# Optimization experiments

Hardware: AMD Instinct MI355X
Metric: run time of the kernel (lower is better)

Reference implementation:

```python
import jax, jax.numpy as jnp
import numpy as np

N_SERIES = 100000
INPUT_SIZE = 28
OUTPUT_SIZE = 7
N_T = 1
N_S = 4
PERIOD = 7            # seasonality = [7]
EMBED = 1 + 1 + PERIOD  # lev_sms, seas_sms, init seasonal factors
BATCH = 2048
N_TIME = 2048


def setup_inputs() -> dict:
    key = jax.random.key(0)
    k1, k2, k3, k4 = jax.random.split(key, 4)
    # Y must be strictly positive (multiplicative model: division + log)
    Y = jax.random.uniform(k1, (BATCH, N_TIME), dtype=jnp.float32, minval=0.5, maxval=1.5)
    X = jax.random.normal(k2, (BATCH, N_T, N_TIME), dtype=jnp.float32)
    S = jax.random.normal(k3, (BATCH, N_S), dtype=jnp.float32)
    idxs = jax.random.randint(k4, (BATCH,), 0, N_SERIES)
    embeds_weight = jnp.full((N_SERIES, EMBED), 0.5, dtype=jnp.float32)
    return {"S": S, "Y": Y, "X": X, "idxs": idxs,
            "embeds_weight": embeds_weight, "step_size": 7}


def _levels_seasons(Y, idxs, embeds_weight):
    """Exponential smoothing level/seasonality recurrence (single seasonality)."""
    emb = embeds_weight[idxs]                      # (B, 9)
    lev_sms = jax.nn.sigmoid(emb[:, 0])            # (B,)
    seas_sms = jax.nn.sigmoid(emb[:, 1])           # (B,)
    init_seas = jnp.exp(emb[:, 2:2 + PERIOD])      # (B, 7)

    level0 = Y[:, 0] / init_seas[:, 0]
    # ring buffer holding the seasonal factors used at steps t=1..: [s1..s6, s0]
    buf0 = jnp.concatenate([init_seas[:, 1:], init_seas[:, :1]], axis=1)  # (B, 7)

    def step(carry, inp):
        lev, buf = carry
        y, k = inp
        s = jnp.take(buf, k % PERIOD, axis=1)                       # seasonality at lag PERIOD
        newlev = lev_sms * (y / s) + (1.0 - lev_sms) * lev
        news = seas_sms * (y / newlev) + (1.0 - seas_sms) * s
        buf = jax.lax.dynamic_update_slice_in_dim(buf, news[:, None], k % PERIOD, axis=1)
        return (newlev, buf), (newlev, news)

    ks = jnp.arange(N_TIME - 1, dtype=jnp.int32)
    (_, _), (levs, seas) = jax.lax.scan(step, (level0, buf0), (Y[:, 1:].T, ks))
    levels = jnp.concatenate([level0[:, None], levs.T], axis=1)           # (B, n_time)
    seasonal = jnp.concatenate([init_seas, init_seas[:, :1], seas.T], axis=1)  # (B, n_time+7)
    return levels, seasonal


def reference(S, Y, X, idxs, embeds_weight, step_size):
    levels, seasonal = _levels_seasons(Y, idxs, embeds_weight)

    windows_end = N_TIME - INPUT_SIZE - OUTPUT_SIZE + 1
    windows = np.arange(0, windows_end, step_size)          # static window starts
    W = len(windows)

    # --- insample windows, normalized: log(Y / level / season) ---
    idx_in = windows[:, None] + np.arange(INPUT_SIZE)       # (W, I)
    Yw = Y[:, idx_in]                                       # (B, W, I)
    lev_w = levels[:, windows + INPUT_SIZE - 1]             # (B, W)
    seas_w = seasonal[:, idx_in]                            # (B, W, I)
    y_in = jnp.log(Yw / (lev_w[:, :, None] * seas_w))
    y_in = y_in.transpose(1, 0, 2)                          # (W, B, I)

    # --- exogenous windows: X[:, :, start:start+I+O].reshape(B, -1) ---
    idx_x = windows[:, None] + np.arange(INPUT_SIZE + OUTPUT_SIZE)  # (W, I+O)
    Xw = X[:, :, idx_x].transpose(2, 0, 1, 3).reshape(W, BATCH, N_T * (INPUT_SIZE + OUTPUT_SIZE))

    # --- static features ---
    Sw = jnp.broadcast_to(S[None], (W, BATCH, N_S))

    windows_y_insample = jnp.concatenate([y_in, Xw, Sw], axis=2)   # (W, B, context)

    # --- outsample windows (eval mode: not normalized) ---
    idx_out = windows[:, None] + INPUT_SIZE + np.arange(OUTPUT_SIZE)  # (W, O)
    windows_y_outsample = Y[:, idx_out].transpose(1, 0, 2)            # (W, B, O)

    return windows_y_insample, windows_y_outsample, levels, seasonal
```

## Files before the change

### kernel.cpp

```cpp
#include <hip/hip_runtime.h>
#include <math.h>

#define BATCH 2048
#define N_TIME 2048
#define INPUT_SIZE 28
#define OUTPUT_SIZE 7
#define N_S 4
#define PERIOD 7
#define EMBED 9
#define SEAS_LEN (N_TIME + PERIOD)
#define W_COUNT 288
#define WB_COUNT (W_COUNT * BATCH)
#define INS_COLS 67
#define OUT0_SIZE (WB_COUNT * INS_COLS)
#define OUT1_SIZE (WB_COUNT * OUTPUT_SIZE)
#define LEV_SIZE (BATCH * N_TIME)
#define SEAS_SIZE (BATCH * SEAS_LEN)

struct ScanState {
    float lev, lsms, seas_sms, oma, oms;
    float sbuf[PERIOD];
    float rbuf[PERIOD];
    float yp, sp, rnlp, rnsp;
};

template<bool FIRST, bool LAST, bool PREF>
__device__ __forceinline__ void scan_chunk(
    int base, int l,
    const float* __restrict__ Yb,
    float (&cur)[64], float (&nxt)[64],
    float (*__restrict__ tl)[65], float (*__restrict__ ts)[65],
    ScanState& st)
{
    if (PREF) {
#pragma unroll
        for (int k = 0; k < 64; k += 4)
            *(float4*)&nxt[k] = *(const float4*)(Yb + base + 64 + k);
    }
    tl[l][0] = st.lev;
#pragma unroll
    for (int k = 0; k < 64; ++k) {
        if (!LAST || k < 63) {
            float y  = (k < 63) ? cur[k + 1] : nxt[0];
            float s0 = st.sbuf[0];
            float nl = fmaf(st.oma, st.lev, y * st.rbuf[0]);
            st.lev = nl;
            tl[l][k + 1] = nl;
            if (!FIRST || k > 0) {
                float u  = st.yp * st.rnlp;
                float ns = fmaf(st.oms, st.sp, st.seas_sms * u);
                ts[l][k] = ns;
                st.sbuf[PERIOD - 1] = ns;
                if (!FIRST || k > 1)
                    st.rbuf[PERIOD - 2] = st.lsms * st.rnsp;
                st.rnsp = __builtin_amdgcn_rcpf(ns);
            }
            float rnl = __builtin_amdgcn_rcpf(nl);
#pragma unroll
            for (int q = 0; q < PERIOD - 1; ++q) st.sbuf[q] = st.sbuf[q + 1];
#pragma unroll
            for (int q = 0; q < PERIOD - 1; ++q) st.rbuf[q] = st.rbuf[q + 1];
            st.yp = y; st.sp = s0; st.rnlp = rnl;
        }
    }
    if (LAST) {
        float u  = st.yp * st.rnlp;
        float ns = fmaf(st.oms, st.sp, st.seas_sms * u);
        ts[l][63] = ns;
    }
    asm volatile("s_waitcnt lgkmcnt(0)" ::: "memory");
    __builtin_amdgcn_s_barrier();
}

__device__ __forceinline__ void drain_chunk(
    int base, int jr, int km, int r0,
    const float (*__restrict__ tl)[65], const float (*__restrict__ ts)[65],
    float* __restrict__ levels, float* __restrict__ seasonal)
{
    __builtin_amdgcn_s_barrier();
    asm volatile("" ::: "memory");
#pragma unroll
    for (int j0 = 0; j0 < 64; j0 += 4) {
        int j = j0 + jr;
        float vl[4], vs[4];
#pragma unroll
        for (int i = 0; i < 4; ++i) { vl[i] = tl[j][km + i]; vs[i] = ts[j][km + i]; }
        float4 v4; v4.x = vl[0]; v4.y = vl[1]; v4.z = vl[2]; v4.w = vl[3];
        *(float4*)(levels + (size_t)(r0 + j) * N_TIME + base + km) = v4;
        float* srow = seasonal + (size_t)(r0 + j) * SEAS_LEN + base + 7 + km;
#pragma unroll
        for (int i = 0; i < 4; ++i) srow[i] = vs[i];
    }
    asm volatile("s_waitcnt lgkmcnt(0)" ::: "memory");
}

__global__ __launch_bounds__(128) void es_scan(
    const float* __restrict__ Y, const int* __restrict__ idxs,
    const float* __restrict__ emb,
    float* __restrict__ levels, float* __restrict__ seasonal)
{
    __shared__ float tl[2][64][65];
    __shared__ float ts[2][64][65];
    const int tid = threadIdx.x;
    const int l   = tid & 63;
    const int r0  = blockIdx.x * 64;

    if (tid < 64) {
        const int b = r0 + l;
        const float* Yb = Y + (size_t)b * N_TIME;
        const float* e  = emb + (size_t)idxs[b] * EMBED;
        ScanState st;
        st.lsms     = 1.0f / (1.0f + __expf(-e[0]));
        st.seas_sms = 1.0f / (1.0f + __expf(-e[1]));
        st.oma = 1.0f - st.lsms;
        st.oms = 1.0f - st.seas_sms;
        float is[PERIOD];
#pragma unroll
        for (int j = 0; j < PERIOD; ++j) is[j] = __expf(e[2 + j]);
        st.lev = Yb[0] / is[0];

        float* seab = seasonal + (size_t)b * SEAS_LEN;
#pragma unroll
        for (int j = 0; j < PERIOD; ++j) seab[j] = is[j];
        ts[0][l][0] = is[0];
#pragma unroll
        for (int j = 0; j < PERIOD; ++j) st.sbuf[j] = is[(j + 1) % PERIOD];
#pragma unroll
        for (int j = 0; j < PERIOD; ++j)
            st.rbuf[j] = st.lsms * __builtin_amdgcn_rcpf(st.sbuf[j]);
        st.yp = 0.0f; st.sp = 1.0f; st.rnlp = 1.0f; st.rnsp = 1.0f;

        float ya[64], yb2[64];
#pragma unroll
        for (int k = 0; k < 64; k += 4)
            *(float4*)&ya[k] = *(const float4*)(Yb + k);

        scan_chunk<true,  false, true >(0, l, Yb, ya, yb2, tl[0], ts[0], st);
#pragma unroll 1
        for (int cc = 0; cc < 15; ++cc) {
            scan_chunk<false, false, true>(64  + cc * 128, l, Yb, yb2, ya, tl[1], ts[1], st);
            scan_chunk<false, false, true>(128 + cc * 128, l, Yb, ya, yb2, tl[0], ts[0], st);
        }
        scan_chunk<false, true,  false>(1984, l, Yb, yb2, ya, tl[1], ts[1], st);
    } else {
        const int jr = l >> 4;
        const int km = (l & 15) * 4;
#pragma unroll 1
        for (int c = 0; c < 32; ++c)
            drain_chunk(c * 64, jr, km, r0, tl[c & 1], ts[c & 1], levels, seasonal);
    }
}

__global__ __launch_bounds__(256) void es_windows(
    const float* __restrict__ Y, const float* __restrict__ X,
    const float* __restrict__ S, const float* __restrict__ levels,
    const float* __restrict__ seasonal,
    float* __restrict__ out0, float* __restrict__ out1)
{
    int gid = blockIdx.x * 256 + threadIdx.x;
    if (gid < OUT0_SIZE) {
        unsigned u  = (unsigned)gid;
        unsigned wb = u / 67u;
        int j  = (int)(u - wb * 67u);
        int w  = (int)(wb >> 11);
        int b  = (int)(wb & (BATCH - 1));
        int t0 = w * 7;
        float v;
        if (j < INPUT_SIZE) {
            float y  = Y[b * N_TIME + t0 + j];
            float lv = levels[b * N_TIME + t0 + INPUT_SIZE - 1];
            float sv = seasonal[b * SEAS_LEN + t0 + j];
            v = __logf(y * __builtin_amdgcn_rcpf(lv * sv));
        } else if (j < 63) {
            v = X[b * N_TIME + t0 + (j - INPUT_SIZE)];
        } else {
            v = S[b * N_S + (j - 63)];
        }
        out0[gid] = v;
    } else {
        unsigned e  = (unsigned)(gid - OUT0_SIZE);
        unsigned wb = e / 7u;
        int m  = (int)(e - wb * 7u);
        int w  = (int)(wb >> 11);
        int b  = (int)(wb & (BATCH - 1));
        out1[e] = Y[b * N_TIME + w * 7 + INPUT_SIZE + m];
    }
}

extern "C" void kernel_launch(void* const* d_in, const int* in_sizes, int n_in,
                              void* d_out, int out_size, void* d_ws, size_t ws_size,
                              hipStream_t stream) {
    const float* S    = (const float*)d_in[0];
    const float* Y    = (const float*)d_in[1];
    const float* X    = (const float*)d_in[2];
    const int*   idxs = (const int*)d_in[3];
    const float* emb  = (const float*)d_in[4];

    float* out      = (float*)d_out;
    float* out_ins  = out;
    float* out_outs = out + OUT0_SIZE;
    float* levels   = out + OUT0_SIZE + OUT1_SIZE;
    float* seasonal = out + OUT0_SIZE + OUT1_SIZE + LEV_SIZE;

    es_scan<<<BATCH / 64, 128, 0, stream>>>(Y, idxs, emb, levels, seasonal);

    const int total = OUT0_SIZE + OUT1_SIZE;
    es_windows<<<total / 256, 256, 0, stream>>>(
        Y, X, S, levels, seasonal, out_ins, out_outs);
}
```

Measured before the change: 356.5 us.

## Overlap scan-independent window copies with the sequential scan kernel

The exogenous X/S window columns and the outsample Y windows do not depend on levels or seasonal. They are now written by extra blocks launched alongside the 32 latency-bound scan blocks in the same kernel. The second kernel only computes the 28 normalized log columns per window. The idea is to hide a large share of the memory-bound copy traffic under the long serial scan, at the cost of strided partial-row writes into out0 and possible contention with the scan blocks.

Result: slower. 463.3 us (+30.0%).

```diff
diff --git a/kernel.cpp b/kernel.cpp
--- a/kernel.cpp
+++ b/kernel.cpp
@@ -16,6 +16,12 @@
 #define OUT1_SIZE (WB_COUNT * OUTPUT_SIZE)
 #define LEV_SIZE (BATCH * N_TIME)
 #define SEAS_SIZE (BATCH * SEAS_LEN)
+
+#define M0_COPY (WB_COUNT * 39)
+#define M_COPY  (M0_COPY + OUT1_SIZE)
+#define COPY_BLOCKS 480
+#define GRID1 (32 + COPY_BLOCKS)
+#define N_YIN (WB_COUNT * INPUT_SIZE)
 
 struct ScanState {
     float lev, lsms, seas_sms, oma, oms;
@@ -94,17 +100,57 @@
     asm volatile("s_waitcnt lgkmcnt(0)" ::: "memory");
 }
 
-__global__ __launch_bounds__(128) void es_scan(
+__device__ __forceinline__ void copy_elem(
+    unsigned g,
+    const float* __restrict__ Y, const float* __restrict__ X,
+    const float* __restrict__ S,
+    float* __restrict__ out0, float* __restrict__ out1)
+{
+    if (g < M0_COPY) {
+        unsigned wb = g / 39u;
+        int jj = (int)(g - wb * 39u);
+        int w  = (int)(wb >> 11);
+        int b  = (int)(wb & (BATCH - 1));
+        float v = (jj < 35) ? X[b * N_TIME + w * 7 + jj]
+                            : S[b * N_S + (jj - 35)];
+        out0[(size_t)wb * 67u + 28u + (unsigned)jj] = v;
+    } else {
+        unsigned e  = g - M0_COPY;
+        unsigned wb = e / 7u;
+        int m  = (int)(e - wb * 7u);
+        int w  = (int)(wb >> 11);
+        int b  = (int)(wb & (BATCH - 1));
+        out1[e] = Y[b * N_TIME + w * 7 + INPUT_SIZE + m];
+    }
+}
+
+__global__ __launch_bounds__(128) void es_scan_plus(
     const float* __restrict__ Y, const int* __restrict__ idxs,
-    const float* __restrict__ emb,
-    float* __restrict__ levels, float* __restrict__ seasonal)
+    const float* __restrict__ emb, const float* __restrict__ X,
+    const float* __restrict__ S,
+    float* __restrict__ levels, float* __restrict__ seasonal,
+    float* __restrict__ out0, float* __restrict__ out1)
 {
     __shared__ float tl[2][64][65];
     __shared__ float ts[2][64][65];
     const int tid = threadIdx.x;
     const int l   = tid & 63;
-    const int r0  = blockIdx.x * 64;
-
+
+    if (blockIdx.x >= 32) {
+        const unsigned stride = COPY_BLOCKS * 128;
+        unsigned g0 = (blockIdx.x - 32) * 128 + tid;
+#pragma unroll 1
+        for (unsigned g = g0; g < M_COPY; g += stride * 4) {
+#pragma unroll
+            for (int u = 0; u < 4; ++u) {
+                unsigned gg = g + (unsigned)u * stride;
+                if (gg < M_COPY) copy_elem(gg, Y, X, S, out0, out1);
+            }
+        }
+        return;
+    }
+
+    const int r0 = blockIdx.x * 64;
     if (tid < 64) {
         const int b = r0 + l;
         const float* Yb = Y + (size_t)b * N_TIME;
@@ -151,40 +197,21 @@
     }
 }
 
-__global__ __launch_bounds__(256) void es_windows(
-    const float* __restrict__ Y, const float* __restrict__ X,
-    const float* __restrict__ S, const float* __restrict__ levels,
-    const float* __restrict__ seasonal,
-    float* __restrict__ out0, float* __restrict__ out1)
-{
-    int gid = blockIdx.x * 256 + threadIdx.x;
-    if (gid < OUT0_SIZE) {
-        unsigned u  = (unsigned)gid;
-        unsigned wb = u / 67u;
-        int j  = (int)(u - wb * 67u);
-        int w  = (int)(wb >> 11);
-        int b  = (int)(wb & (BATCH - 1));
-        int t0 = w * 7;
-        float v;
-        if (j < INPUT_SIZE) {
-            float y  = Y[b * N_TIME + t0 + j];
-            float lv = levels[b * N_TIME + t0 + INPUT_SIZE - 1];
-            float sv = seasonal[b * SEAS_LEN + t0 + j];
-            v = __logf(y * __builtin_amdgcn_rcpf(lv * sv));
-        } else if (j < 63) {
-            v = X[b * N_TIME + t0 + (j - INPUT_SIZE)];
-        } else {
-            v = S[b * N_S + (j - 63)];
-        }
-        out0[gid] = v;
-    } else {
-        unsigned e  = (unsigned)(gid - OUT0_SIZE);
-        unsigned wb = e / 7u;
-        int m  = (int)(e - wb * 7u);
-        int w  = (int)(wb >> 11);
-        int b  = (int)(wb & (BATCH - 1));
-        out1[e] = Y[b * N_TIME + w * 7 + INPUT_SIZE + m];
-    }
+__global__ __launch_bounds__(256) void es_windows_yin(
+    const float* __restrict__ Y, const float* __restrict__ levels,
+    const float* __restrict__ seasonal, float* __restrict__ out0)
+{
+    unsigned gid = blockIdx.x * 256 + threadIdx.x;
+    unsigned wb = gid / 28u;
+    int j  = (int)(gid - wb * 28u);
+    int w  = (int)(wb >> 11);
+    int b  = (int)(wb & (BATCH - 1));
+    int t0 = w * 7;
+    float y  = Y[b * N_TIME + t0 + j];
+    float lv = levels[b * N_TIME + t0 + INPUT_SIZE - 1];
+    float sv = seasonal[b * SEAS_LEN + t0 + j];
+    out0[(size_t)wb * 67u + (unsigned)j] =
+        __logf(y * __builtin_amdgcn_rcpf(lv * sv));
 }
 
 extern "C" void kernel_launch(void* const* d_in, const int* in_sizes, int n_in,
@@ -202,9 +229,9 @@
     float* levels   = out + OUT0_SIZE + OUT1_SIZE;
     float* seasonal = out + OUT0_SIZE + OUT1_SIZE + LEV_SIZE;
 
-    es_scan<<<BATCH / 64, 128, 0, stream>>>(Y, idxs, emb, levels, seasonal);
-
-    const int total = OUT0_SIZE + OUT1_SIZE;
-    es_windows<<<total / 256, 256, 0, stream>>>(
-        Y, X, S, levels, seasonal, out_ins, out_outs);
-}
+    es_scan_plus<<<GRID1, 128, 0, stream>>>(
+        Y, idxs, emb, X, S, levels, seasonal, out_ins, out_outs);
+
+    es_windows_yin<<<N_YIN / 256, 256, 0, stream>>>(
+        Y, levels, seasonal, out_ins);
+}
```
